# Performance work log

Measured on AMD Instinct MI355X. Metric: run time of the kernel, lower is better.

The kernel has to match this reference:

```python
import jax, jax.numpy as jnp
import numpy as np

IGNORE_INDEX = -100


def setup_inputs() -> dict:
    key = jax.random.key(0)
    k1, k2, k3 = jax.random.split(key, 3)
    BT, H, V = 4096, 2048, 32000
    hidden_states = jax.random.normal(k1, (BT, H), dtype=jnp.float32) * 0.02
    weight = jax.random.normal(k2, (V, H), dtype=jnp.float32) * 0.02
    targets = jax.random.randint(k3, (BT,), 0, V, dtype=jnp.int64)
    return {"hidden_states": hidden_states, "weight": weight, "targets": targets}


def reference(hidden_states, weight, targets):
    # Fused lm_head projection + cross-entropy with ignore_index masking,
    # 'mean' reduction over valid rows (matches reduction='mean').
    logits = jnp.einsum('bh,vh->bv', hidden_states, weight).astype(jnp.float32)  # (BT, V)
    lse = jax.nn.logsumexp(logits, axis=-1)  # (BT,)
    safe_tgt = jnp.clip(targets, 0, logits.shape[-1] - 1)
    target_logit = jnp.take_along_axis(logits, safe_tgt[:, None], axis=-1)[:, 0]
    valid = targets != IGNORE_INDEX
    loss_rows = jnp.where(valid, lse - target_logit, 0.0)  # (BT,)
    n_valid = jnp.maximum(valid.sum(), 1)
    return loss_rows.sum() / n_valid.astype(jnp.float32)
```

## Files before the change

### kernel.cpp

```cpp
#include <hip/hip_runtime.h>

#define BT 4096
#define H  2048
#define V  32000
#define BM 256
#define BN 256
#define BKB 128
#define KT (H / BKB)
#define NTILES (V / BN)
#define MTILES (BT / BM)
#define NWG (MTILES * NTILES)
#define IGNORE_INDEX (-100)

typedef int   v8i   __attribute__((ext_vector_type(8)));
typedef float f32x4 __attribute__((ext_vector_type(4)));

#define SCALE_ONE 0x7F7F7F7F
#define UNSCALE   (1.0f / 65536.0f)

#define BAR()   __builtin_amdgcn_s_barrier()
#define LGKM0() asm volatile("s_waitcnt lgkmcnt(0)" ::: "memory")
#define LGKM8() asm volatile("s_waitcnt lgkmcnt(8)" ::: "memory")
#define VMC(N)  asm volatile("s_waitcnt vmcnt(" #N ")" ::: "memory")

__device__ inline void load_lds16(const void* g, void* l) {
  __builtin_amdgcn_global_load_lds(
      (const __attribute__((address_space(1))) unsigned int*)g,
      (__attribute__((address_space(3))) unsigned int*)l,
      16, 0, 0);
}

__global__ __launch_bounds__(256)
void cvt_pack_kernel(const float* __restrict__ in, unsigned char* __restrict__ out,
                     int tasks) {
  int task = blockIdx.x * 4 + (threadIdx.x >> 6);
  if (task >= tasks) return;
  const int g    = task >> 4;
  const int kt   = task & 15;
  const int lane = threadIdx.x & 63;
  const float* src = in + (size_t)(g * 16 + (lane & 15)) * H
                        + kt * 128 + (lane >> 4) * 32;
  int p[8];
#pragma unroll
  for (int u = 0; u < 8; ++u) {
    float4 x = ((const float4*)src)[u];
    int v = 0;
    v = __builtin_amdgcn_cvt_pk_fp8_f32(x.x * 256.f, x.y * 256.f, v, false);
    v = __builtin_amdgcn_cvt_pk_fp8_f32(x.z * 256.f, x.w * 256.f, v, true);
    p[u] = v;
  }
  unsigned char* dst = out + ((size_t)g * KT + kt) * 2048 + lane * 16;
  int4 lo; lo.x = p[0]; lo.y = p[1]; lo.z = p[2]; lo.w = p[3];
  int4 hi; hi.x = p[4]; hi.y = p[5]; hi.z = p[6]; hi.w = p[7];
  *(int4*)dst          = lo;
  *(int4*)(dst + 1024) = hi;
}

union frag_u { v8i v; int4 h[2]; };

#define MF(C, A, B)                                                         \
  (C) = __builtin_amdgcn_mfma_scale_f32_16x16x128_f8f6f4(                   \
      (A).v, (B).v, (C), 0, 0, 0, SCALE_ONE, 0, SCALE_ONE)

__global__ __launch_bounds__(512, 2)
void gemm_lse_kernel(const unsigned char* __restrict__ Af8,
                     const unsigned char* __restrict__ Bf8,
                     const int* __restrict__ tgt,
                     float* __restrict__ pm, float* __restrict__ pl,
                     float* __restrict__ tl) {
  __shared__ __align__(16) unsigned char As[2 * 32768];
  __shared__ __align__(16) unsigned char Bs[2 * 32768];
  __shared__ float red_m[4][BM];
  __shared__ float red_l[4][BM];
  __shared__ int   stgt[BM];

  const int wgid = ((int)blockIdx.x & 7) * (NWG / 8) + ((int)blockIdx.x >> 3);
  const int mt = wgid & (MTILES - 1);
  const int nt = wgid / MTILES;
  const int m0 = mt * BM;
  const int n0 = nt * BN;

  const int tid  = threadIdx.x;
  const int lane = tid & 63;
  const int w    = tid >> 6;
  const int wr   = w >> 2;
  const int wc   = w & 3;
  const int lm   = lane & 15;
  const int q    = lane >> 4;

  if (tid < BM) stgt[tid] = tgt[m0 + tid];
  __syncthreads();

  const unsigned char* aSrc = Af8 + (size_t)(m0 / 16) * KT * 2048;
  const unsigned char* bSrc = Bf8 + (size_t)(n0 / 16) * KT * 2048;

  auto stageA = [&](int buf, int hf, int kt) {
    const unsigned char* s = aSrc + ((size_t)(hf * 8 + w) * KT + kt) * 2048;
    unsigned char* d = As + buf * 32768 + (hf * 8 + w) * 2048;
    load_lds16(s, d);
    load_lds16(s + 1024, d + 1024);
  };
  auto stageB = [&](int buf, int hf, int kt) {
    const unsigned char* s = bSrc + ((size_t)(hf * 8 + w) * KT + kt) * 2048;
    unsigned char* d = Bs + buf * 32768 + (hf * 8 + w) * 2048;
    load_lds16(s, d);
    load_lds16(s + 1024, d + 1024);
  };

  const unsigned char* aRd = As + lane * 16;
  const unsigned char* bRd = Bs + lane * 16;

  auto ldA = [&](frag_u& f, int buf, int i) {
    const unsigned char* p = aRd + buf * 32768 + (wr * 8 + i) * 2048;
    f.h[0] = *(const int4*)(p);
    f.h[1] = *(const int4*)(p + 1024);
  };
  auto ldB = [&](frag_u& f, int buf, int j) {
    const unsigned char* p = bRd + buf * 32768 + (wc * 4 + j) * 2048;
    f.h[0] = *(const int4*)(p);
    f.h[1] = *(const int4*)(p + 1024);
  };

  f32x4 acc[8][4];
#pragma unroll
  for (int a = 0; a < 8; ++a)
#pragma unroll
    for (int b = 0; b < 4; ++b) acc[a][b] = (f32x4){0.f, 0.f, 0.f, 0.f};

  frag_u fa0, fa1, fa2, fa3, fb0, fb1, fb2, fb3;

  stageA(0, 0, 0); stageA(0, 1, 0); stageB(0, 0, 0); stageB(0, 1, 0);
  stageB(1, 0, 1); stageB(1, 1, 1);
  VMC(4);
  BAR();

  for (int i = 0; i < 8; ++i) {
    const int t0 = 2 * i, t1 = 2 * i + 1;
    const bool pre = (i < 7);

    ldA(fa0, 0, 0); ldA(fa1, 0, 1); ldA(fa2, 0, 2); ldA(fa3, 0, 3);
    ldB(fb0, 0, 0); ldB(fb1, 0, 1);
    stageA(1, 0, t1);
    LGKM8();
    BAR(); LGKM0();
    __builtin_amdgcn_s_setprio(1);
    MF(acc[0][0], fa0, fb0); MF(acc[1][0], fa1, fb0);
    MF(acc[2][0], fa2, fb0); MF(acc[3][0], fa3, fb0);
    MF(acc[0][1], fa0, fb1); MF(acc[1][1], fa1, fb1);
    MF(acc[2][1], fa2, fb1); MF(acc[3][1], fa3, fb1);
    __builtin_amdgcn_s_setprio(0);
    BAR();

    ldB(fb2, 0, 2); ldB(fb3, 0, 3);
    stageA(1, 1, t1);
    BAR(); LGKM0();
    __builtin_amdgcn_s_setprio(1);
    MF(acc[0][2], fa0, fb2); MF(acc[1][2], fa1, fb2);
    MF(acc[2][2], fa2, fb2); MF(acc[3][2], fa3, fb2);
    MF(acc[0][3], fa0, fb3); MF(acc[1][3], fa1, fb3);
    MF(acc[2][3], fa2, fb3); MF(acc[3][3], fa3, fb3);
    __builtin_amdgcn_s_setprio(0);
    BAR();

    ldA(fa0, 0, 4); ldA(fa1, 0, 5); ldA(fa2, 0, 6); ldA(fa3, 0, 7);
    if (pre) stageB(0, 0, t0 + 2);
    BAR(); LGKM0();
    __builtin_amdgcn_s_setprio(1);
    MF(acc[4][0], fa0, fb0); MF(acc[5][0], fa1, fb0);
    MF(acc[6][0], fa2, fb0); MF(acc[7][0], fa3, fb0);
    MF(acc[4][1], fa0, fb1); MF(acc[5][1], fa1, fb1);
    MF(acc[6][1], fa2, fb1); MF(acc[7][1], fa3, fb1);
    __builtin_amdgcn_s_setprio(0);
    BAR();

    if (pre) stageB(0, 1, t0 + 2);
    BAR(); LGKM0();
    __builtin_amdgcn_s_setprio(1);
    MF(acc[4][2], fa0, fb2); MF(acc[5][2], fa1, fb2);
    MF(acc[6][2], fa2, fb2); MF(acc[7][2], fa3, fb2);
    MF(acc[4][3], fa0, fb3); MF(acc[5][3], fa1, fb3);
    MF(acc[6][3], fa2, fb3); MF(acc[7][3], fa3, fb3);
    __builtin_amdgcn_s_setprio(0);
    if (pre) { VMC(4); } else { VMC(0); }
    BAR();

    ldA(fa0, 1, 0); ldA(fa1, 1, 1); ldA(fa2, 1, 2); ldA(fa3, 1, 3);
    ldB(fb0, 1, 0); ldB(fb1, 1, 1);
    if (pre) stageA(0, 0, t0 + 2);
    LGKM8();
    BAR(); LGKM0();
    __builtin_amdgcn_s_setprio(1);
    MF(acc[0][0], fa0, fb0); MF(acc[1][0], fa1, fb0);
    MF(acc[2][0], fa2, fb0); MF(acc[3][0], fa3, fb0);
    MF(acc[0][1], fa0, fb1); MF(acc[1][1], fa1, fb1);
    MF(acc[2][1], fa2, fb1); MF(acc[3][1], fa3, fb1);
    __builtin_amdgcn_s_setprio(0);
    BAR();

    ldB(fb2, 1, 2); ldB(fb3, 1, 3);
    if (pre) stageA(0, 1, t0 + 2);
    BAR(); LGKM0();
    __builtin_amdgcn_s_setprio(1);
    MF(acc[0][2], fa0, fb2); MF(acc[1][2], fa1, fb2);
    MF(acc[2][2], fa2, fb2); MF(acc[3][2], fa3, fb2);
    MF(acc[0][3], fa0, fb3); MF(acc[1][3], fa1, fb3);
    MF(acc[2][3], fa2, fb3); MF(acc[3][3], fa3, fb3);
    __builtin_amdgcn_s_setprio(0);
    BAR();

    ldA(fa0, 1, 4); ldA(fa1, 1, 5); ldA(fa2, 1, 6); ldA(fa3, 1, 7);
    if (pre) stageB(1, 0, t1 + 2);
    BAR(); LGKM0();
    __builtin_amdgcn_s_setprio(1);
    MF(acc[4][0], fa0, fb0); MF(acc[5][0], fa1, fb0);
    MF(acc[6][0], fa2, fb0); MF(acc[7][0], fa3, fb0);
    MF(acc[4][1], fa0, fb1); MF(acc[5][1], fa1, fb1);
    MF(acc[6][1], fa2, fb1); MF(acc[7][1], fa3, fb1);
    __builtin_amdgcn_s_setprio(0);
    BAR();

    if (pre) stageB(1, 1, t1 + 2);
    BAR(); LGKM0();
    __builtin_amdgcn_s_setprio(1);
    MF(acc[4][2], fa0, fb2); MF(acc[5][2], fa1, fb2);
    MF(acc[6][2], fa2, fb2); MF(acc[7][2], fa3, fb2);
    MF(acc[4][3], fa0, fb3); MF(acc[5][3], fa1, fb3);
    MF(acc[6][3], fa2, fb3); MF(acc[7][3], fa3, fb3);
    __builtin_amdgcn_s_setprio(0);
    if (pre) { VMC(4); } else { VMC(0); }
    BAR();
  }

  __syncthreads();

#pragma unroll
  for (int ai = 0; ai < 8; ++ai) {
#pragma unroll
    for (int r = 0; r < 4; ++r) {
      int row_local = wr * 128 + ai * 16 + q * 4 + r;
      int c = stgt[row_local] - n0 - wc * 64;
      if ((unsigned)c < 64u && (c & 15) == lm) {
        int bj = c >> 4;
        float v = bj == 0 ? acc[ai][0][r]
                : bj == 1 ? acc[ai][1][r]
                : bj == 2 ? acc[ai][2][r]
                :           acc[ai][3][r];
        tl[m0 + row_local] = v * UNSCALE;
      }
    }
  }

#pragma unroll
  for (int ai = 0; ai < 8; ++ai) {
#pragma unroll
    for (int r = 0; r < 4; ++r) {
      float v0 = acc[ai][0][r] * UNSCALE;
      float v1 = acc[ai][1][r] * UNSCALE;
      float v2 = acc[ai][2][r] * UNSCALE;
      float v3 = acc[ai][3][r] * UNSCALE;
      float mx = fmaxf(fmaxf(v0, v1), fmaxf(v2, v3));
#pragma unroll
      for (int off = 1; off < 16; off <<= 1) mx = fmaxf(mx, __shfl_xor(mx, off));
      float s = __expf(v0 - mx) + __expf(v1 - mx) + __expf(v2 - mx) + __expf(v3 - mx);
#pragma unroll
      for (int off = 1; off < 16; off <<= 1) s += __shfl_xor(s, off);
      if (lm == 0) {
        int row_local = wr * 128 + ai * 16 + q * 4 + r;
        red_m[wc][row_local] = mx;
        red_l[wc][row_local] = s;
      }
    }
  }
  __syncthreads();
  if (tid < BM) {
    float M = fmaxf(fmaxf(red_m[0][tid], red_m[1][tid]),
                    fmaxf(red_m[2][tid], red_m[3][tid]));
    float L = red_l[0][tid] * __expf(red_m[0][tid] - M)
            + red_l[1][tid] * __expf(red_m[1][tid] - M)
            + red_l[2][tid] * __expf(red_m[2][tid] - M)
            + red_l[3][tid] * __expf(red_m[3][tid] - M);
    long idx = (long)nt * BT + (m0 + tid);
    pm[idx] = M;
    pl[idx] = L;
  }
}

__global__ __launch_bounds__(256)
void row_lse_kernel(const float* __restrict__ pm, const float* __restrict__ pl,
                    const float* __restrict__ tl, const int* __restrict__ tgt,
                    float* __restrict__ rl) {
  int row  = blockIdx.x * 4 + (threadIdx.x >> 6);
  int lane = threadIdx.x & 63;
  float M = -__builtin_inff();
  float L = 0.f;
  for (int t = lane; t < NTILES; t += 64) {
    float m2 = pm[(long)t * BT + row];
    float l2 = pl[(long)t * BT + row];
    float Mn = fmaxf(M, m2);
    L = L * __expf(M - Mn) + l2 * __expf(m2 - Mn);
    M = Mn;
  }
#pragma unroll
  for (int off = 1; off < 64; off <<= 1) {
    float m2 = __shfl_xor(M, off);
    float l2 = __shfl_xor(L, off);
    float Mn = fmaxf(M, m2);
    L = L * __expf(M - Mn) + l2 * __expf(m2 - Mn);
    M = Mn;
  }
  if (lane == 0) {
    float lse = M + logf(L);
    int t = tgt[row];
    rl[row] = (t != IGNORE_INDEX) ? (lse - tl[row]) : 0.f;
  }
}

__global__ __launch_bounds__(256)
void final_kernel(const float* __restrict__ rl, const int* __restrict__ tgt,
                  float* __restrict__ out) {
  __shared__ float ss[4];
  __shared__ float sc[4];
  float s = 0.f, c = 0.f;
  for (int r = threadIdx.x; r < BT; r += 256) {
    s += rl[r];
    c += (tgt[r] != IGNORE_INDEX) ? 1.f : 0.f;
  }
#pragma unroll
  for (int off = 32; off > 0; off >>= 1) {
    s += __shfl_xor(s, off);
    c += __shfl_xor(c, off);
  }
  int w = threadIdx.x >> 6;
  if ((threadIdx.x & 63) == 0) { ss[w] = s; sc[w] = c; }
  __syncthreads();
  if (threadIdx.x == 0) {
    float S = ss[0] + ss[1] + ss[2] + ss[3];
    float C = sc[0] + sc[1] + sc[2] + sc[3];
    out[0] = S / fmaxf(C, 1.f);
  }
}

extern "C" void kernel_launch(void* const* d_in, const int* in_sizes, int n_in,
                              void* d_out, int out_size, void* d_ws, size_t ws_size,
                              hipStream_t stream) {
  const float* hs  = (const float*)d_in[0];
  const float* wt  = (const float*)d_in[1];
  const int*   tgt = (const int*)d_in[2];
  float*       out = (float*)d_out;

  char* ws = (char*)d_ws;
  size_t off = 0;
  auto alloc = [&](size_t bytes) -> void* {
    void* p = ws + off;
    off += (bytes + 255) & ~(size_t)255;
    return p;
  };
  unsigned char* wf8 = (unsigned char*)alloc((size_t)V * H);
  unsigned char* hf8 = (unsigned char*)alloc((size_t)BT * H);
  float* pm = (float*)alloc((size_t)NTILES * BT * 4);
  float* pl = (float*)alloc((size_t)NTILES * BT * 4);
  float* tl = (float*)alloc((size_t)BT * 4);
  float* rl = (float*)alloc((size_t)BT * 4);
  (void)ws_size; (void)in_sizes; (void)n_in; (void)out_size;

  cvt_pack_kernel<<<(V / 16) * KT / 4, 256, 0, stream>>>(wt, wf8, (V / 16) * KT);
  cvt_pack_kernel<<<(BT / 16) * KT / 4, 256, 0, stream>>>(hs, hf8, (BT / 16) * KT);

  gemm_lse_kernel<<<NWG, 512, 0, stream>>>(hf8, wf8, tgt, pm, pl, tl);

  row_lse_kernel<<<BT / 4, 256, 0, stream>>>(pm, pl, tl, tgt, rl);
  final_kernel<<<1, 256, 0, stream>>>(rl, tgt, out);
}
```

Baseline: 709.5 us.

## Load A fragments directly to registers and stage B through register prefetch

The GEMM kernel stops staging A through shared memory. Each wave now loads its A fragments straight from global memory into registers, while B goes through registers and is written into a double-buffered LDS array. This replaces the async global_load_lds pipeline with far fewer barriers per k-step, and the tile order changes to m-major. The conversion kernel now stages each 16x128 block through LDS so its global reads are coalesced. Risks include extra register pressure, A loads no longer shared across the workgroup (more global and L2 traffic), and exposed global latency, since the loop waits on lgkm but not explicitly on vmcnt.

```diff
diff --git a/kernel.cpp b/kernel.cpp
--- a/kernel.cpp
+++ b/kernel.cpp
@@ -20,30 +20,29 @@
 
 #define BAR()   __builtin_amdgcn_s_barrier()
 #define LGKM0() asm volatile("s_waitcnt lgkmcnt(0)" ::: "memory")
-#define LGKM8() asm volatile("s_waitcnt lgkmcnt(8)" ::: "memory")
-#define VMC(N)  asm volatile("s_waitcnt vmcnt(" #N ")" ::: "memory")
-
-__device__ inline void load_lds16(const void* g, void* l) {
-  __builtin_amdgcn_global_load_lds(
-      (const __attribute__((address_space(1))) unsigned int*)g,
-      (__attribute__((address_space(3))) unsigned int*)l,
-      16, 0, 0);
-}
 
 __global__ __launch_bounds__(256)
 void cvt_pack_kernel(const float* __restrict__ in, unsigned char* __restrict__ out,
                      int tasks) {
-  int task = blockIdx.x * 4 + (threadIdx.x >> 6);
+  __shared__ float ld[4][16][132];
+  const int wv = threadIdx.x >> 6, lane = threadIdx.x & 63;
+  const int task = blockIdx.x * 4 + wv;
   if (task >= tasks) return;
-  const int g    = task >> 4;
-  const int kt   = task & 15;
-  const int lane = threadIdx.x & 63;
-  const float* src = in + (size_t)(g * 16 + (lane & 15)) * H
-                        + kt * 128 + (lane >> 4) * 32;
+  const int g = task >> 4, kt = task & 15;
+  const float* src = in + (size_t)(g * 16) * H + kt * 128;
+#pragma unroll
+  for (int i = 0; i < 8; ++i) {
+    int idx = i * 64 + lane;
+    int r = idx >> 5, c = idx & 31;
+    float4 v = *(const float4*)(src + (size_t)r * H + c * 4);
+    *(float4*)&ld[wv][r][c * 4] = v;
+  }
+  LGKM0();
+  const int row = lane & 15, kb = (lane >> 4) * 32;
   int p[8];
 #pragma unroll
   for (int u = 0; u < 8; ++u) {
-    float4 x = ((const float4*)src)[u];
+    float4 x = *(const float4*)&ld[wv][row][kb + u * 4];
     int v = 0;
     v = __builtin_amdgcn_cvt_pk_fp8_f32(x.x * 256.f, x.y * 256.f, v, false);
     v = __builtin_amdgcn_cvt_pk_fp8_f32(x.z * 256.f, x.w * 256.f, v, true);
@@ -68,15 +67,14 @@
                      const int* __restrict__ tgt,
                      float* __restrict__ pm, float* __restrict__ pl,
                      float* __restrict__ tl) {
-  __shared__ __align__(16) unsigned char As[2 * 32768];
   __shared__ __align__(16) unsigned char Bs[2 * 32768];
   __shared__ float red_m[4][BM];
   __shared__ float red_l[4][BM];
   __shared__ int   stgt[BM];
 
   const int wgid = ((int)blockIdx.x & 7) * (NWG / 8) + ((int)blockIdx.x >> 3);
-  const int mt = wgid & (MTILES - 1);
-  const int nt = wgid / MTILES;
+  const int mt = wgid / NTILES;
+  const int nt = wgid % NTILES;
   const int m0 = mt * BM;
   const int n0 = nt * BN;
 
@@ -91,35 +89,42 @@
   if (tid < BM) stgt[tid] = tgt[m0 + tid];
   __syncthreads();
 
-  const unsigned char* aSrc = Af8 + (size_t)(m0 / 16) * KT * 2048;
-  const unsigned char* bSrc = Bf8 + (size_t)(n0 / 16) * KT * 2048;
-
-  auto stageA = [&](int buf, int hf, int kt) {
-    const unsigned char* s = aSrc + ((size_t)(hf * 8 + w) * KT + kt) * 2048;
-    unsigned char* d = As + buf * 32768 + (hf * 8 + w) * 2048;
-    load_lds16(s, d);
-    load_lds16(s + 1024, d + 1024);
-  };
-  auto stageB = [&](int buf, int hf, int kt) {
-    const unsigned char* s = bSrc + ((size_t)(hf * 8 + w) * KT + kt) * 2048;
-    unsigned char* d = Bs + buf * 32768 + (hf * 8 + w) * 2048;
-    load_lds16(s, d);
-    load_lds16(s + 1024, d + 1024);
-  };
-
-  const unsigned char* aRd = As + lane * 16;
-  const unsigned char* bRd = Bs + lane * 16;
-
-  auto ldA = [&](frag_u& f, int buf, int i) {
-    const unsigned char* p = aRd + buf * 32768 + (wr * 8 + i) * 2048;
+  const unsigned char* aSrc =
+      Af8 + ((size_t)(m0 / 16 + wr * 8) * KT) * 2048 + lane * 16;
+  const unsigned char* bSrc =
+      Bf8 + ((size_t)(n0 / 16 + 2 * w) * KT) * 2048 + lane * 16;
+
+  frag_u a03[4], a47[4];
+  int4 bst[4];
+
+  auto loadA = [&](frag_u* f, int kt2, int half) {
+    int k = kt2 < KT ? kt2 : KT - 1;
+    const unsigned char* p = aSrc + ((size_t)(half * 4) * KT + k) * 2048;
+#pragma unroll
+    for (int i = 0; i < 4; ++i) {
+      f[i].h[0] = *(const int4*)(p + (size_t)i * KT * 2048);
+      f[i].h[1] = *(const int4*)(p + (size_t)i * KT * 2048 + 1024);
+    }
+  };
+  auto bload = [&](int kt2) {
+    int k = kt2 < KT ? kt2 : KT - 1;
+    bst[0] = *(const int4*)(bSrc + (size_t)k * 2048);
+    bst[1] = *(const int4*)(bSrc + (size_t)k * 2048 + 1024);
+    bst[2] = *(const int4*)(bSrc + ((size_t)KT + k) * 2048);
+    bst[3] = *(const int4*)(bSrc + ((size_t)KT + k) * 2048 + 1024);
+  };
+  auto bwrite = [&](int buf) {
+    unsigned char* d = Bs + buf * 32768 + (2 * w) * 2048 + lane * 16;
+    *(int4*)(d)        = bst[0];
+    *(int4*)(d + 1024) = bst[1];
+    *(int4*)(d + 2048) = bst[2];
+    *(int4*)(d + 3072) = bst[3];
+  };
+  auto ldsB = [&](frag_u& f, int buf, int j) {
+    const unsigned char* p = Bs + buf * 32768 + (wc * 4 + j) * 2048 + lane * 16;
     f.h[0] = *(const int4*)(p);
     f.h[1] = *(const int4*)(p + 1024);
   };
-  auto ldB = [&](frag_u& f, int buf, int j) {
-    const unsigned char* p = bRd + buf * 32768 + (wc * 4 + j) * 2048;
-    f.h[0] = *(const int4*)(p);
-    f.h[1] = *(const int4*)(p + 1024);
-  };
 
   f32x4 acc[8][4];
 #pragma unroll
@@ -127,107 +132,55 @@
 #pragma unroll
     for (int b = 0; b < 4; ++b) acc[a][b] = (f32x4){0.f, 0.f, 0.f, 0.f};
 
-  frag_u fa0, fa1, fa2, fa3, fb0, fb1, fb2, fb3;
-
-  stageA(0, 0, 0); stageA(0, 1, 0); stageB(0, 0, 0); stageB(0, 1, 0);
-  stageB(1, 0, 1); stageB(1, 1, 1);
-  VMC(4);
+  bload(0);
+  loadA(a03, 0, 0);
+  loadA(a47, 0, 1);
+  bwrite(0);
+  LGKM0();
   BAR();
-
-  for (int i = 0; i < 8; ++i) {
-    const int t0 = 2 * i, t1 = 2 * i + 1;
-    const bool pre = (i < 7);
-
-    ldA(fa0, 0, 0); ldA(fa1, 0, 1); ldA(fa2, 0, 2); ldA(fa3, 0, 3);
-    ldB(fb0, 0, 0); ldB(fb1, 0, 1);
-    stageA(1, 0, t1);
-    LGKM8();
-    BAR(); LGKM0();
+  bload(1);
+
+#pragma unroll 2
+  for (int kt = 0; kt < KT; ++kt) {
+    const int buf = kt & 1;
+    frag_u fbA, fbB;
+
+    ldsB(fbA, buf, 0); ldsB(fbB, buf, 1);
     __builtin_amdgcn_s_setprio(1);
-    MF(acc[0][0], fa0, fb0); MF(acc[1][0], fa1, fb0);
-    MF(acc[2][0], fa2, fb0); MF(acc[3][0], fa3, fb0);
-    MF(acc[0][1], fa0, fb1); MF(acc[1][1], fa1, fb1);
-    MF(acc[2][1], fa2, fb1); MF(acc[3][1], fa3, fb1);
+    MF(acc[0][0], a03[0], fbA); MF(acc[1][0], a03[1], fbA);
+    MF(acc[2][0], a03[2], fbA); MF(acc[3][0], a03[3], fbA);
+    MF(acc[0][1], a03[0], fbB); MF(acc[1][1], a03[1], fbB);
+    MF(acc[2][1], a03[2], fbB); MF(acc[3][1], a03[3], fbB);
     __builtin_amdgcn_s_setprio(0);
-    BAR();
-
-    ldB(fb2, 0, 2); ldB(fb3, 0, 3);
-    stageA(1, 1, t1);
-    BAR(); LGKM0();
+
+    ldsB(fbA, buf, 2); ldsB(fbB, buf, 3);
     __builtin_amdgcn_s_setprio(1);
-    MF(acc[0][2], fa0, fb2); MF(acc[1][2], fa1, fb2);
-    MF(acc[2][2], fa2, fb2); MF(acc[3][2], fa3, fb2);
-    MF(acc[0][3], fa0, fb3); MF(acc[1][3], fa1, fb3);
-    MF(acc[2][3], fa2, fb3); MF(acc[3][3], fa3, fb3);
+    MF(acc[0][2], a03[0], fbA); MF(acc[1][2], a03[1], fbA);
+    MF(acc[2][2], a03[2], fbA); MF(acc[3][2], a03[3], fbA);
+    MF(acc[0][3], a03[0], fbB); MF(acc[1][3], a03[1], fbB);
+    MF(acc[2][3], a03[2], fbB); MF(acc[3][3], a03[3], fbB);
     __builtin_amdgcn_s_setprio(0);
-    BAR();
-
-    ldA(fa0, 0, 4); ldA(fa1, 0, 5); ldA(fa2, 0, 6); ldA(fa3, 0, 7);
-    if (pre) stageB(0, 0, t0 + 2);
-    BAR(); LGKM0();
+
+    loadA(a03, kt + 1, 0);
+    bwrite(buf ^ 1);
+    ldsB(fbA, buf, 0); ldsB(fbB, buf, 1);
     __builtin_amdgcn_s_setprio(1);
-    MF(acc[4][0], fa0, fb0); MF(acc[5][0], fa1, fb0);
-    MF(acc[6][0], fa2, fb0); MF(acc[7][0], fa3, fb0);
-    MF(acc[4][1], fa0, fb1); MF(acc[5][1], fa1, fb1);
-    MF(acc[6][1], fa2, fb1); MF(acc[7][1], fa3, fb1);
+    MF(acc[4][0], a47[0], fbA); MF(acc[5][0], a47[1], fbA);
+    MF(acc[6][0], a47[2], fbA); MF(acc[7][0], a47[3], fbA);
+    MF(acc[4][1], a47[0], fbB); MF(acc[5][1], a47[1], fbB);
+    MF(acc[6][1], a47[2], fbB); MF(acc[7][1], a47[3], fbB);
     __builtin_amdgcn_s_setprio(0);
-    BAR();
-
-    if (pre) stageB(0, 1, t0 + 2);
-    BAR(); LGKM0();
+
+    ldsB(fbA, buf, 2); ldsB(fbB, buf, 3);
     __builtin_amdgcn_s_setprio(1);
-    MF(acc[4][2], fa0, fb2); MF(acc[5][2], fa1, fb2);
-    MF(acc[6][2], fa2, fb2); MF(acc[7][2], fa3, fb2);
-    MF(acc[4][3], fa0, fb3); MF(acc[5][3], fa1, fb3);
-    MF(acc[6][3], fa2, fb3); MF(acc[7][3], fa3, fb3);
+    MF(acc[4][2], a47[0], fbA); MF(acc[5][2], a47[1], fbA);
+    MF(acc[6][2], a47[2], fbA); MF(acc[7][2], a47[3], fbA);
+    MF(acc[4][3], a47[0], fbB); MF(acc[5][3], a47[1], fbB);
+    MF(acc[6][3], a47[2], fbB); MF(acc[7][3], a47[3], fbB);
     __builtin_amdgcn_s_setprio(0);
-    if (pre) { VMC(4); } else { VMC(0); }
-    BAR();
-
-    ldA(fa0, 1, 0); ldA(fa1, 1, 1); ldA(fa2, 1, 2); ldA(fa3, 1, 3);
-    ldB(fb0, 1, 0); ldB(fb1, 1, 1);
-    if (pre) stageA(0, 0, t0 + 2);
-    LGKM8();
-    BAR(); LGKM0();
-    __builtin_amdgcn_s_setprio(1);
-    MF(acc[0][0], fa0, fb0); MF(acc[1][0], fa1, fb0);
-    MF(acc[2][0], fa2, fb0); MF(acc[3][0], fa3, fb0);
-    MF(acc[0][1], fa0, fb1); MF(acc[1][1], fa1, fb1);
-    MF(acc[2][1], fa2, fb1); MF(acc[3][1], fa3, fb1);
-    __builtin_amdgcn_s_setprio(0);
-    BAR();
-
-    ldB(fb2, 1, 2); ldB(fb3, 1, 3);
-    if (pre) stageA(0, 1, t0 + 2);
-    BAR(); LGKM0();
-    __builtin_amdgcn_s_setprio(1);
-    MF(acc[0][2], fa0, fb2); MF(acc[1][2], fa1, fb2);
-    MF(acc[2][2], fa2, fb2); MF(acc[3][2], fa3, fb2);
-    MF(acc[0][3], fa0, fb3); MF(acc[1][3], fa1, fb3);
-    MF(acc[2][3], fa2, fb3); MF(acc[3][3], fa3, fb3);
-    __builtin_amdgcn_s_setprio(0);
-    BAR();
-
-    ldA(fa0, 1, 4); ldA(fa1, 1, 5); ldA(fa2, 1, 6); ldA(fa3, 1, 7);
-    if (pre) stageB(1, 0, t1 + 2);
-    BAR(); LGKM0();
-    __builtin_amdgcn_s_setprio(1);
-    MF(acc[4][0], fa0, fb0); MF(acc[5][0], fa1, fb0);
-    MF(acc[6][0], fa2, fb0); MF(acc[7][0], fa3, fb0);
-    MF(acc[4][1], fa0, fb1); MF(acc[5][1], fa1, fb1);
-    MF(acc[6][1], fa2, fb1); MF(acc[7][1], fa3, fb1);
-    __builtin_amdgcn_s_setprio(0);
-    BAR();
-
-    if (pre) stageB(1, 1, t1 + 2);
-    BAR(); LGKM0();
-    __builtin_amdgcn_s_setprio(1);
-    MF(acc[4][2], fa0, fb2); MF(acc[5][2], fa1, fb2);
-    MF(acc[6][2], fa2, fb2); MF(acc[7][2], fa3, fb2);
-    MF(acc[4][3], fa0, fb3); MF(acc[5][3], fa1, fb3);
-    MF(acc[6][3], fa2, fb3); MF(acc[7][3], fa3, fb3);
-    __builtin_amdgcn_s_setprio(0);
-    if (pre) { VMC(4); } else { VMC(0); }
+    loadA(a47, kt + 1, 1);
+    bload(kt + 2);
+    LGKM0();
     BAR();
   }
 
```

New measurement: 942.5 us. 1.33x slower.

## Halve GEMM main-loop barriers and stage fp8 pack through LDS for coalescing

Applied to the files above, without the earlier changes.

The FP8 GEMM main loop merges pairs of 8-MFMA phases into 16-MFMA phases. This halves the number of workgroup barriers and LDS waits per K step, and the B fragments and both A-stage halves are issued together. Scheduling barriers are placed around each s_barrier to stop the compiler from moving memory ops across them. The fp32-to-fp8 pack kernel now loads rows coalesced into LDS before converting, instead of using strided per-lane reads. In exchange, register pressure rises (all four B fragments are live at once), and the explicit LDS wait before the barrier is dropped, so correctness depends on the compiler's waitcnt insertion.

```diff
diff --git a/kernel.cpp b/kernel.cpp
--- a/kernel.cpp
+++ b/kernel.cpp
@@ -19,8 +19,8 @@
 #define UNSCALE   (1.0f / 65536.0f)
 
 #define BAR()   __builtin_amdgcn_s_barrier()
+#define SB0()   __builtin_amdgcn_sched_barrier(0)
 #define LGKM0() asm volatile("s_waitcnt lgkmcnt(0)" ::: "memory")
-#define LGKM8() asm volatile("s_waitcnt lgkmcnt(8)" ::: "memory")
 #define VMC(N)  asm volatile("s_waitcnt vmcnt(" #N ")" ::: "memory")
 
 __device__ inline void load_lds16(const void* g, void* l) {
@@ -33,17 +33,25 @@
 __global__ __launch_bounds__(256)
 void cvt_pack_kernel(const float* __restrict__ in, unsigned char* __restrict__ out,
                      int tasks) {
-  int task = blockIdx.x * 4 + (threadIdx.x >> 6);
+  __shared__ float ld[4][16][132];
+  const int wv = threadIdx.x >> 6, lane = threadIdx.x & 63;
+  const int task = blockIdx.x * 4 + wv;
   if (task >= tasks) return;
-  const int g    = task >> 4;
-  const int kt   = task & 15;
-  const int lane = threadIdx.x & 63;
-  const float* src = in + (size_t)(g * 16 + (lane & 15)) * H
-                        + kt * 128 + (lane >> 4) * 32;
+  const int g = task >> 4, kt = task & 15;
+  const float* src = in + (size_t)(g * 16) * H + kt * 128;
+#pragma unroll
+  for (int i = 0; i < 8; ++i) {
+    int idx = i * 64 + lane;
+    int r = idx >> 5, c = idx & 31;
+    float4 v = *(const float4*)(src + (size_t)r * H + c * 4);
+    *(float4*)&ld[wv][r][c * 4] = v;
+  }
+  LGKM0();
+  const int row = lane & 15, kb = (lane >> 4) * 32;
   int p[8];
 #pragma unroll
   for (int u = 0; u < 8; ++u) {
-    float4 x = ((const float4*)src)[u];
+    float4 x = *(const float4*)&ld[wv][row][kb + u * 4];
     int v = 0;
     v = __builtin_amdgcn_cvt_pk_fp8_f32(x.x * 256.f, x.y * 256.f, v, false);
     v = __builtin_amdgcn_cvt_pk_fp8_f32(x.z * 256.f, x.w * 256.f, v, true);
@@ -132,103 +140,71 @@
   stageA(0, 0, 0); stageA(0, 1, 0); stageB(0, 0, 0); stageB(0, 1, 0);
   stageB(1, 0, 1); stageB(1, 1, 1);
   VMC(4);
-  BAR();
+  SB0(); BAR(); SB0();
 
   for (int i = 0; i < 8; ++i) {
-    const int t0 = 2 * i, t1 = 2 * i + 1;
+    const int t1 = 2 * i + 1;
     const bool pre = (i < 7);
 
     ldA(fa0, 0, 0); ldA(fa1, 0, 1); ldA(fa2, 0, 2); ldA(fa3, 0, 3);
-    ldB(fb0, 0, 0); ldB(fb1, 0, 1);
-    stageA(1, 0, t1);
-    LGKM8();
-    BAR(); LGKM0();
+    ldB(fb0, 0, 0); ldB(fb1, 0, 1); ldB(fb2, 0, 2); ldB(fb3, 0, 3);
+    stageA(1, 0, t1); stageA(1, 1, t1);
     __builtin_amdgcn_s_setprio(1);
     MF(acc[0][0], fa0, fb0); MF(acc[1][0], fa1, fb0);
     MF(acc[2][0], fa2, fb0); MF(acc[3][0], fa3, fb0);
     MF(acc[0][1], fa0, fb1); MF(acc[1][1], fa1, fb1);
     MF(acc[2][1], fa2, fb1); MF(acc[3][1], fa3, fb1);
-    __builtin_amdgcn_s_setprio(0);
-    BAR();
-
-    ldB(fb2, 0, 2); ldB(fb3, 0, 3);
-    stageA(1, 1, t1);
-    BAR(); LGKM0();
-    __builtin_amdgcn_s_setprio(1);
     MF(acc[0][2], fa0, fb2); MF(acc[1][2], fa1, fb2);
     MF(acc[2][2], fa2, fb2); MF(acc[3][2], fa3, fb2);
     MF(acc[0][3], fa0, fb3); MF(acc[1][3], fa1, fb3);
     MF(acc[2][3], fa2, fb3); MF(acc[3][3], fa3, fb3);
     __builtin_amdgcn_s_setprio(0);
-    BAR();
+    SB0(); BAR(); SB0();
 
     ldA(fa0, 0, 4); ldA(fa1, 0, 5); ldA(fa2, 0, 6); ldA(fa3, 0, 7);
-    if (pre) stageB(0, 0, t0 + 2);
-    BAR(); LGKM0();
+    if (pre) { stageB(0, 0, 2 * i + 2); stageB(0, 1, 2 * i + 2); }
     __builtin_amdgcn_s_setprio(1);
     MF(acc[4][0], fa0, fb0); MF(acc[5][0], fa1, fb0);
     MF(acc[6][0], fa2, fb0); MF(acc[7][0], fa3, fb0);
     MF(acc[4][1], fa0, fb1); MF(acc[5][1], fa1, fb1);
     MF(acc[6][1], fa2, fb1); MF(acc[7][1], fa3, fb1);
-    __builtin_amdgcn_s_setprio(0);
-    BAR();
-
-    if (pre) stageB(0, 1, t0 + 2);
-    BAR(); LGKM0();
-    __builtin_amdgcn_s_setprio(1);
     MF(acc[4][2], fa0, fb2); MF(acc[5][2], fa1, fb2);
     MF(acc[6][2], fa2, fb2); MF(acc[7][2], fa3, fb2);
     MF(acc[4][3], fa0, fb3); MF(acc[5][3], fa1, fb3);
     MF(acc[6][3], fa2, fb3); MF(acc[7][3], fa3, fb3);
     __builtin_amdgcn_s_setprio(0);
     if (pre) { VMC(4); } else { VMC(0); }
-    BAR();
+    SB0(); BAR(); SB0();
 
     ldA(fa0, 1, 0); ldA(fa1, 1, 1); ldA(fa2, 1, 2); ldA(fa3, 1, 3);
-    ldB(fb0, 1, 0); ldB(fb1, 1, 1);
-    if (pre) stageA(0, 0, t0 + 2);
-    LGKM8();
-    BAR(); LGKM0();
+    ldB(fb0, 1, 0); ldB(fb1, 1, 1); ldB(fb2, 1, 2); ldB(fb3, 1, 3);
+    if (pre) { stageA(0, 0, 2 * i + 2); stageA(0, 1, 2 * i + 2); }
     __builtin_amdgcn_s_setprio(1);
     MF(acc[0][0], fa0, fb0); MF(acc[1][0], fa1, fb0);
     MF(acc[2][0], fa2, fb0); MF(acc[3][0], fa3, fb0);
     MF(acc[0][1], fa0, fb1); MF(acc[1][1], fa1, fb1);
     MF(acc[2][1], fa2, fb1); MF(acc[3][1], fa3, fb1);
-    __builtin_amdgcn_s_setprio(0);
-    BAR();
-
-    ldB(fb2, 1, 2); ldB(fb3, 1, 3);
-    if (pre) stageA(0, 1, t0 + 2);
-    BAR(); LGKM0();
-    __builtin_amdgcn_s_setprio(1);
     MF(acc[0][2], fa0, fb2); MF(acc[1][2], fa1, fb2);
     MF(acc[2][2], fa2, fb2); MF(acc[3][2], fa3, fb2);
     MF(acc[0][3], fa0, fb3); MF(acc[1][3], fa1, fb3);
     MF(acc[2][3], fa2, fb3); MF(acc[3][3], fa3, fb3);
     __builtin_amdgcn_s_setprio(0);
-    BAR();
+    SB0(); BAR(); SB0();
 
     ldA(fa0, 1, 4); ldA(fa1, 1, 5); ldA(fa2, 1, 6); ldA(fa3, 1, 7);
-    if (pre) stageB(1, 0, t1 + 2);
-    BAR(); LGKM0();
+    if (pre) { stageB(1, 0, t1 + 2); stageB(1, 1, t1 + 2); }
     __builtin_amdgcn_s_setprio(1);
     MF(acc[4][0], fa0, fb0); MF(acc[5][0], fa1, fb0);
     MF(acc[6][0], fa2, fb0); MF(acc[7][0], fa3, fb0);
     MF(acc[4][1], fa0, fb1); MF(acc[5][1], fa1, fb1);
     MF(acc[6][1], fa2, fb1); MF(acc[7][1], fa3, fb1);
-    __builtin_amdgcn_s_setprio(0);
-    BAR();
-
-    if (pre) stageB(1, 1, t1 + 2);
-    BAR(); LGKM0();
-    __builtin_amdgcn_s_setprio(1);
     MF(acc[4][2], fa0, fb2); MF(acc[5][2], fa1, fb2);
     MF(acc[6][2], fa2, fb2); MF(acc[7][2], fa3, fb2);
     MF(acc[4][3], fa0, fb3); MF(acc[5][3], fa1, fb3);
     MF(acc[6][3], fa2, fb3); MF(acc[7][3], fa3, fb3);
     __builtin_amdgcn_s_setprio(0);
     if (pre) { VMC(4); } else { VMC(0); }
-    BAR();
+    SB0(); BAR(); SB0();
   }
 
   __syncthreads();
```

Measured after the change: 724.0 us. +2.1%, slower.
